# Performance work log

Hardware: AMD Instinct MI355X
Metric: run time of the kernel (lower is better)

The kernel has to match this reference:

```python
import jax, jax.numpy as jnp
import numpy as np

N, C, H, W = 32, 49, 9, 9   # batch, spectral bands (=outplane), spatial patch
MSIZE, K, PAD = 24, 7, 3    # conv3d out channels, spectral kernel, padding
EPS = 1e-5


def setup_inputs() -> dict:
    key = jax.random.key(0)
    k1, k2, k3 = jax.random.split(key, 3)
    x = jax.random.normal(k1, (N, C, H, W), dtype=jnp.float32)
    # Conv3d(1, MSIZE, [7,1,1]) params, PyTorch default uniform init
    fan_in = 1 * K * 1 * 1
    bound = 1.0 / np.sqrt(fan_in)
    conv_w = jax.random.uniform(k2, (MSIZE, 1, K, 1, 1), jnp.float32, -bound, bound)
    conv_b = jax.random.uniform(k3, (MSIZE,), jnp.float32, -bound, bound)
    # BatchNorm2d(49) affine params at init
    gamma = jnp.ones((C,), jnp.float32)
    beta = jnp.zeros((C,), jnp.float32)
    return {"x": x, "conv_w": conv_w, "conv_b": conv_b, "gamma": gamma, "beta": beta}


def reference(x, conv_w, conv_b, gamma, beta):
    n, c, h, w = x.shape
    # Conv3d over (depth=spectral, h, w) with kernel [K,1,1]: depth preserved
    x5 = x[:, None]  # (n,1,c,h,w)
    m = jax.lax.conv_general_dilated(
        x5, conv_w, window_strides=(1, 1, 1),
        padding=[(PAD, PAD), (0, 0), (0, 0)],
        dimension_numbers=("NCDHW", "OIDHW", "NCDHW"),
    ) + conv_b[None, :, None, None, None]        # (n, MSIZE, c, h, w)
    d = m.shape[1] * m.shape[2]                   # d = MSIZE * c
    mask = jax.nn.softmax(m.reshape(n, d, h * w), axis=-1).reshape(n, d, h, w)
    # original computes convm0 twice -> mask1 == mask0; reuse `mask` for both
    fk = jnp.einsum("ndhw,nchw->ncd", mask, x)    # (n, c, d)
    # out[n,c,h,w] = sum_d leaky_relu(fk[n,c,d] * mask[n,d,h,w])
    big = jnp.einsum("ncd,ndhw->ncdhw", fk, mask)  # (n,c,d,h,w) large intermediate
    out = jax.nn.leaky_relu(big, negative_slope=0.01).sum(axis=2)
    out = out + x                                  # residual
    # BatchNorm2d in training mode: batch statistics over (n,h,w) per channel
    mean = out.mean(axis=(0, 2, 3))
    var = out.var(axis=(0, 2, 3))
    out = (out - mean[:, None, None]) * jax.lax.rsqrt(var[:, None, None] + EPS)
    out = out * gamma[:, None, None] + beta[:, None, None]
    return out
```

## Files before the change

kernel.cpp:

```cpp
#include <hip/hip_runtime.h>
#include <hip/hip_bf16.h>

#define NN    32
#define CC    49
#define HWSZ  81
#define MSZ   24
#define KSZ   7
#define PADSZ 3
#define NHW   (NN*HWSZ)
#define NCHW  (NN*CC*HWSZ)

#define OPB   3
#define OGRP  (MSZ/OPB)

#define XSB_S  104
#define MSK_S  104
#define MSKT_S 72
#define G_S    72

typedef __attribute__((ext_vector_type(8))) short short8;
typedef __attribute__((ext_vector_type(4))) short short4v;
typedef __attribute__((ext_vector_type(4))) float f32x4;

__device__ __forceinline__ short f2b(float v) {
    unsigned u = __float_as_uint(v);
    u += 0x7fffu + ((u >> 16) & 1u);
    return (short)(u >> 16);
}
__device__ __forceinline__ float b2f(short s) {
    return __uint_as_float(((unsigned)(unsigned short)s) << 16);
}

__global__ __launch_bounds__(512) void fuse_k1(
    const float* __restrict__ x, const float* __restrict__ cw,
    const float* __restrict__ cb, float* __restrict__ acc)
{
    __shared__ short xsb [64 * XSB_S];
    __shared__ short msk [64 * MSK_S];
    __shared__ short mskT[96 * MSKT_S];
    __shared__ short gm  [64 * G_S];

    const int og = blockIdx.x;
    const int n  = blockIdx.y;
    const int t  = threadIdx.x;
    const int lane = t & 63;
    const int wv = t >> 6;
    const int lr = lane & 15;
    const int lq = lane >> 4;

    const float* xg = x + (size_t)n * CC * HWSZ;

    const f32x4 z4 = {0.f, 0.f, 0.f, 0.f};
    for (int i = t; i < CC * HWSZ; i += 512) {
        int c = i / HWSZ, hw = i - c * HWSZ;
        xsb[c * XSB_S + hw] = f2b(xg[i]);
    }
    if (t < CC) {
        short* row = xsb + t * XSB_S;
        #pragma unroll
        for (int cq = 81; cq < 88; ++cq) row[cq] = 0;
        *(f32x4*)(row + 88) = z4;
        *(f32x4*)(row + 96) = z4;
    }
    for (int j = t; j < 15 * 13; j += 512) {
        int rr = j / 13, cg = j - rr * 13;
        *(f32x4*)(xsb + (49 + rr) * XSB_S + cg * 8) = z4;
    }
    for (int i = t; i < 832; i += 512) ((f32x4*)msk)[i] = z4;
    for (int i = t; i < 864; i += 512) ((f32x4*)mskT)[i] = z4;
    __syncthreads();

    const int mt   = wv & 3;
    const int ntc0 = (wv >> 2) * 2;
    const int ct   = wv & 3;
    const int nh   = (wv >> 2) * 3;

    f32x4 dacc[3];
    #pragma unroll
    for (int j = 0; j < 3; ++j) dacc[j] = z4;

    for (int oo = 0; oo < OPB; ++oo) {
        const int o = og * OPB + oo;
        float wk[KSZ];
        #pragma unroll
        for (int k = 0; k < KSZ; ++k) wk[k] = cw[o * KSZ + k];
        const float bias = cb[o];

        #pragma unroll
        for (int it = 0; it < 2; ++it) {
            int dd = it * 32 + wv * 4 + lq;
            if (dd < CC) {
                float a0 = 0.f, a1 = 0.f, a2 = 0.f, a3 = 0.f, a4 = 0.f, a5 = 0.f;
                #pragma unroll
                for (int k = 0; k < KSZ; ++k) {
                    int r = dd + k - PADSZ;
                    if (r >= 0 && r < CC) {
                        const short* xr = xsb + r * XSB_S;
                        short4v xa = *(const short4v*)(xr + 4 * lr);
                        float w = wk[k];
                        a0 += w * b2f(xa[0]);
                        a1 += w * b2f(xa[1]);
                        a2 += w * b2f(xa[2]);
                        a3 += w * b2f(xa[3]);
                        a4 += w * b2f(xr[64 + lr]);
                        if (lr == 0) a5 += w * b2f(xr[80]);
                    }
                }
                float e0 = __expf(a0 + bias), e1 = __expf(a1 + bias);
                float e2 = __expf(a2 + bias), e3 = __expf(a3 + bias);
                float e4 = __expf(a4 + bias);
                float e5 = (lr == 0) ? __expf(a5 + bias) : 0.f;
                float s = ((e0 + e1) + (e2 + e3)) + (e4 + e5);
                #pragma unroll
                for (int off = 8; off; off >>= 1) s += __shfl_xor(s, off, 64);
                float inv = __builtin_amdgcn_rcpf(s);
                short4v pk;
                pk[0] = f2b(e0 * inv); pk[1] = f2b(e1 * inv);
                pk[2] = f2b(e2 * inv); pk[3] = f2b(e3 * inv);
                short b4 = f2b(e4 * inv);
                short* mrow = msk + dd * MSK_S;
                *(short4v*)(mrow + 4 * lr) = pk;
                mrow[64 + lr] = b4;
                mskT[(4 * lr    ) * MSKT_S + dd] = pk[0];
                mskT[(4 * lr + 1) * MSKT_S + dd] = pk[1];
                mskT[(4 * lr + 2) * MSKT_S + dd] = pk[2];
                mskT[(4 * lr + 3) * MSKT_S + dd] = pk[3];
                mskT[(64 + lr   ) * MSKT_S + dd] = b4;
                if (lr == 0) {
                    short b5 = f2b(e5 * inv);
                    mrow[80] = b5;
                    mskT[80 * MSKT_S + dd] = b5;
                }
            }
        }
        __syncthreads();

        {
            short8 a2f[3];
            #pragma unroll
            for (int ks = 0; ks < 3; ++ks)
                a2f[ks] = *(const short8*)&msk[(mt * 16 + lr) * MSK_S + ks * 32 + lq * 8];
            #pragma unroll
            for (int jn = 0; jn < 2; ++jn) {
                int nt = ntc0 + jn;
                f32x4 accv = {0.f, 0.f, 0.f, 0.f};
                #pragma unroll
                for (int ks = 0; ks < 3; ++ks) {
                    short8 b = *(const short8*)&xsb[(nt * 16 + lr) * XSB_S + ks * 32 + lq * 8];
                    accv = __builtin_amdgcn_mfma_f32_16x16x32_bf16(a2f[ks], b, accv, 0, 0, 0);
                }
                short4v pk;
                #pragma unroll
                for (int r = 0; r < 4; ++r) {
                    float v = accv[r];
                    v = (v >= 0.f) ? v : 0.01f * v;
                    pk[r] = f2b(v);
                }
                *(short4v*)&gm[(nt * 16 + lr) * G_S + mt * 16 + lq * 4] = pk;
            }
        }
        __syncthreads();

        {
            short8 a1f[2];
            #pragma unroll
            for (int ks = 0; ks < 2; ++ks)
                a1f[ks] = *(const short8*)&gm[(ct * 16 + lr) * G_S + ks * 32 + lq * 8];
            #pragma unroll
            for (int j = 0; j < 3; ++j) {
                int nt = nh + j;
                #pragma unroll
                for (int ks = 0; ks < 2; ++ks) {
                    short8 b = *(const short8*)&mskT[(nt * 16 + lr) * MSKT_S + ks * 32 + lq * 8];
                    dacc[j] = __builtin_amdgcn_mfma_f32_16x16x32_bf16(a1f[ks], b, dacc[j], 0, 0, 0);
                }
            }
        }
        __syncthreads();
    }

    float* dstn = acc + (size_t)n * CC * HWSZ;
    #pragma unroll
    for (int j = 0; j < 3; ++j) {
        int hw = (nh + j) * 16 + lr;
        if (hw < HWSZ) {
            int c0 = ct * 16 + lq * 4;
            #pragma unroll
            for (int r = 0; r < 4; ++r) {
                int c = c0 + r;
                if (c < CC) atomicAdd(dstn + c * HWSZ + hw, dacc[j][r]);
            }
        }
    }
}

__global__ __launch_bounds__(1024) void fuse_k2(
    float* __restrict__ out, const float* __restrict__ x,
    const float* __restrict__ gamma, const float* __restrict__ beta)
{
    const int c = blockIdx.x;
    const int t = threadIdx.x;
    float vals[3];
    float sum = 0.f, sq = 0.f;
    int cnt = 0;
    for (int i = t; i < NHW; i += 1024) {
        int n = i / HWSZ;
        int hw = i - n * HWSZ;
        int idx = (n * CC + c) * HWSZ + hw;
        float v = out[idx] + x[idx];
        vals[cnt++] = v;
        sum += v; sq += v * v;
    }
    #pragma unroll
    for (int off = 32; off; off >>= 1) {
        sum += __shfl_xor(sum, off, 64);
        sq  += __shfl_xor(sq, off, 64);
    }
    __shared__ float rs[16], rq[16];
    const int lane = t & 63, wv = t >> 6;
    if (lane == 0) { rs[wv] = sum; rq[wv] = sq; }
    __syncthreads();
    float ts = 0.f, tq = 0.f;
    #pragma unroll
    for (int w = 0; w < 16; ++w) { ts += rs[w]; tq += rq[w]; }
    const float invD = 1.f / (float)NHW;
    float mean = ts * invD;
    float var  = tq * invD - mean * mean;
    float scal = rsqrtf(var + 1e-5f) * gamma[c];
    float shft = beta[c] - mean * scal;
    cnt = 0;
    for (int i = t; i < NHW; i += 1024) {
        int n = i / HWSZ;
        int hw = i - n * HWSZ;
        out[(n * CC + c) * HWSZ + hw] = vals[cnt++] * scal + shft;
    }
}

extern "C" void kernel_launch(void* const* d_in, const int* in_sizes, int n_in,
                              void* d_out, int out_size, void* d_ws, size_t ws_size,
                              hipStream_t stream) {
    const float* x     = (const float*)d_in[0];
    const float* cw    = (const float*)d_in[1];
    const float* cb    = (const float*)d_in[2];
    const float* gamma = (const float*)d_in[3];
    const float* beta  = (const float*)d_in[4];
    float* out = (float*)d_out;

    hipMemsetAsync(out, 0, (size_t)NCHW * sizeof(float), stream);
    fuse_k1<<<dim3(OGRP, NN), 512, 0, stream>>>(x, cw, cb, out);
    fuse_k2<<<CC, 1024, 0, stream>>>(out, x, gamma, beta);
}
```

Before: 83.31 us.

## Fuse main and batchnorm kernels into one cooperative launch with per-channel blocks

Merges the two kernels into a single cooperative kernel that uses a grid-wide sync between the atomic accumulation and the batch-norm pass. It also changes the work split from 8 groups of 3 output channels with 512 threads to 24 single-channel blocks of 256 threads each. Each block now accumulates its partial result with atomics directly instead of looping over channels in registers. This adds parallelism (768 blocks) and removes one kernel launch, but requires all 768 blocks to be co-resident. It also multiplies atomics by 3 and x loads/conversions by 3, and the BN pass runs on only 49 blocks after the grid sync.

```diff
diff --git a/kernel.cpp b/kernel.cpp
--- a/kernel.cpp
+++ b/kernel.cpp
@@ -1,5 +1,8 @@
 #include <hip/hip_runtime.h>
 #include <hip/hip_bf16.h>
+#include <hip/hip_cooperative_groups.h>
+
+namespace cg = cooperative_groups;
 
 #define NN    32
 #define CC    49
@@ -10,9 +13,6 @@
 #define NHW   (NN*HWSZ)
 #define NCHW  (NN*CC*HWSZ)
 
-#define OPB   3
-#define OGRP  (MSZ/OPB)
-
 #define XSB_S  104
 #define MSK_S  104
 #define MSKT_S 72
@@ -31,27 +31,33 @@
     return __uint_as_float(((unsigned)(unsigned short)s) << 16);
 }
 
-__global__ __launch_bounds__(512) void fuse_k1(
+__global__ __launch_bounds__(256, 3) void fuse_all(
     const float* __restrict__ x, const float* __restrict__ cw,
-    const float* __restrict__ cb, float* __restrict__ acc)
+    const float* __restrict__ cb, const float* __restrict__ gamma,
+    const float* __restrict__ beta, float* __restrict__ out)
 {
     __shared__ short xsb [64 * XSB_S];
     __shared__ short msk [64 * MSK_S];
     __shared__ short mskT[96 * MSKT_S];
     __shared__ short gm  [64 * G_S];
-
-    const int og = blockIdx.x;
-    const int n  = blockIdx.y;
-    const int t  = threadIdx.x;
+    __shared__ float rs[4], rq[4];
+
+    const int o = blockIdx.x;
+    const int n = blockIdx.y;
+    const int t = threadIdx.x;
     const int lane = t & 63;
     const int wv = t >> 6;
     const int lr = lane & 15;
     const int lq = lane >> 4;
 
     const float* xg = x + (size_t)n * CC * HWSZ;
+    float wk[KSZ];
+    #pragma unroll
+    for (int k = 0; k < KSZ; ++k) wk[k] = cw[o * KSZ + k];
+    const float bias = cb[o];
 
     const f32x4 z4 = {0.f, 0.f, 0.f, 0.f};
-    for (int i = t; i < CC * HWSZ; i += 512) {
+    for (int i = t; i < CC * HWSZ; i += 256) {
         int c = i / HWSZ, hw = i - c * HWSZ;
         xsb[c * XSB_S + hw] = f2b(xg[i]);
     }
@@ -62,177 +68,150 @@
         *(f32x4*)(row + 88) = z4;
         *(f32x4*)(row + 96) = z4;
     }
-    for (int j = t; j < 15 * 13; j += 512) {
+    for (int j = t; j < 15 * 13; j += 256) {
         int rr = j / 13, cg = j - rr * 13;
         *(f32x4*)(xsb + (49 + rr) * XSB_S + cg * 8) = z4;
     }
-    for (int i = t; i < 832; i += 512) ((f32x4*)msk)[i] = z4;
-    for (int i = t; i < 864; i += 512) ((f32x4*)mskT)[i] = z4;
+    for (int i = t; i < 832; i += 256) ((f32x4*)msk)[i] = z4;
+    for (int i = t; i < 864; i += 256) ((f32x4*)mskT)[i] = z4;
     __syncthreads();
 
-    const int mt   = wv & 3;
-    const int ntc0 = (wv >> 2) * 2;
-    const int ct   = wv & 3;
-    const int nh   = (wv >> 2) * 3;
-
-    f32x4 dacc[3];
     #pragma unroll
-    for (int j = 0; j < 3; ++j) dacc[j] = z4;
-
-    for (int oo = 0; oo < OPB; ++oo) {
-        const int o = og * OPB + oo;
-        float wk[KSZ];
-        #pragma unroll
-        for (int k = 0; k < KSZ; ++k) wk[k] = cw[o * KSZ + k];
-        const float bias = cb[o];
-
-        #pragma unroll
-        for (int it = 0; it < 2; ++it) {
-            int dd = it * 32 + wv * 4 + lq;
-            if (dd < CC) {
-                float a0 = 0.f, a1 = 0.f, a2 = 0.f, a3 = 0.f, a4 = 0.f, a5 = 0.f;
-                #pragma unroll
-                for (int k = 0; k < KSZ; ++k) {
-                    int r = dd + k - PADSZ;
-                    if (r >= 0 && r < CC) {
-                        const short* xr = xsb + r * XSB_S;
-                        short4v xa = *(const short4v*)(xr + 4 * lr);
-                        float w = wk[k];
-                        a0 += w * b2f(xa[0]);
-                        a1 += w * b2f(xa[1]);
-                        a2 += w * b2f(xa[2]);
-                        a3 += w * b2f(xa[3]);
-                        a4 += w * b2f(xr[64 + lr]);
-                        if (lr == 0) a5 += w * b2f(xr[80]);
-                    }
+    for (int it = 0; it < 4; ++it) {
+        int dd = it * 16 + wv * 4 + lq;
+        if (dd < CC) {
+            float a0 = 0.f, a1 = 0.f, a2 = 0.f, a3 = 0.f, a4 = 0.f, a5 = 0.f;
+            #pragma unroll
+            for (int k = 0; k < KSZ; ++k) {
+                int r = dd + k - PADSZ;
+                if (r >= 0 && r < CC) {
+                    const short* xr = xsb + r * XSB_S;
+                    short4v xa = *(const short4v*)(xr + 4 * lr);
+                    float w = wk[k];
+                    a0 += w * b2f(xa[0]);
+                    a1 += w * b2f(xa[1]);
+                    a2 += w * b2f(xa[2]);
+                    a3 += w * b2f(xa[3]);
+                    a4 += w * b2f(xr[64 + lr]);
+                    if (lr == 0) a5 += w * b2f(xr[80]);
                 }
-                float e0 = __expf(a0 + bias), e1 = __expf(a1 + bias);
-                float e2 = __expf(a2 + bias), e3 = __expf(a3 + bias);
-                float e4 = __expf(a4 + bias);
-                float e5 = (lr == 0) ? __expf(a5 + bias) : 0.f;
-                float s = ((e0 + e1) + (e2 + e3)) + (e4 + e5);
-                #pragma unroll
-                for (int off = 8; off; off >>= 1) s += __shfl_xor(s, off, 64);
-                float inv = __builtin_amdgcn_rcpf(s);
-                short4v pk;
-                pk[0] = f2b(e0 * inv); pk[1] = f2b(e1 * inv);
-                pk[2] = f2b(e2 * inv); pk[3] = f2b(e3 * inv);
-                short b4 = f2b(e4 * inv);
-                short* mrow = msk + dd * MSK_S;
-                *(short4v*)(mrow + 4 * lr) = pk;
-                mrow[64 + lr] = b4;
-                mskT[(4 * lr    ) * MSKT_S + dd] = pk[0];
-                mskT[(4 * lr + 1) * MSKT_S + dd] = pk[1];
-                mskT[(4 * lr + 2) * MSKT_S + dd] = pk[2];
-                mskT[(4 * lr + 3) * MSKT_S + dd] = pk[3];
-                mskT[(64 + lr   ) * MSKT_S + dd] = b4;
-                if (lr == 0) {
-                    short b5 = f2b(e5 * inv);
-                    mrow[80] = b5;
-                    mskT[80 * MSKT_S + dd] = b5;
-                }
-            }
-        }
-        __syncthreads();
-
-        {
-            short8 a2f[3];
-            #pragma unroll
-            for (int ks = 0; ks < 3; ++ks)
-                a2f[ks] = *(const short8*)&msk[(mt * 16 + lr) * MSK_S + ks * 32 + lq * 8];
-            #pragma unroll
-            for (int jn = 0; jn < 2; ++jn) {
-                int nt = ntc0 + jn;
-                f32x4 accv = {0.f, 0.f, 0.f, 0.f};
-                #pragma unroll
-                for (int ks = 0; ks < 3; ++ks) {
-                    short8 b = *(const short8*)&xsb[(nt * 16 + lr) * XSB_S + ks * 32 + lq * 8];
-                    accv = __builtin_amdgcn_mfma_f32_16x16x32_bf16(a2f[ks], b, accv, 0, 0, 0);
-                }
-                short4v pk;
+            }
+            float e0 = __expf(a0 + bias), e1 = __expf(a1 + bias);
+            float e2 = __expf(a2 + bias), e3 = __expf(a3 + bias);
+            float e4 = __expf(a4 + bias);
+            float e5 = (lr == 0) ? __expf(a5 + bias) : 0.f;
+            float s = ((e0 + e1) + (e2 + e3)) + (e4 + e5);
+            #pragma unroll
+            for (int off = 8; off; off >>= 1) s += __shfl_xor(s, off, 64);
+            float inv = __builtin_amdgcn_rcpf(s);
+            short4v pk;
+            pk[0] = f2b(e0 * inv); pk[1] = f2b(e1 * inv);
+            pk[2] = f2b(e2 * inv); pk[3] = f2b(e3 * inv);
+            short b4 = f2b(e4 * inv);
+            short* mrow = msk + dd * MSK_S;
+            *(short4v*)(mrow + 4 * lr) = pk;
+            mrow[64 + lr] = b4;
+            mskT[(4 * lr    ) * MSKT_S + dd] = pk[0];
+            mskT[(4 * lr + 1) * MSKT_S + dd] = pk[1];
+            mskT[(4 * lr + 2) * MSKT_S + dd] = pk[2];
+            mskT[(4 * lr + 3) * MSKT_S + dd] = pk[3];
+            mskT[(64 + lr   ) * MSKT_S + dd] = b4;
+            if (lr == 0) {
+                short b5 = f2b(e5 * inv);
+                mrow[80] = b5;
+                mskT[80 * MSKT_S + dd] = b5;
+            }
+        }
+    }
+    __syncthreads();
+
+    {
+        short8 a2[3];
+        #pragma unroll
+        for (int ks = 0; ks < 3; ++ks)
+            a2[ks] = *(const short8*)&msk[(wv * 16 + lr) * MSK_S + ks * 32 + lq * 8];
+        #pragma unroll
+        for (int nt = 0; nt < 4; ++nt) {
+            f32x4 accv = {0.f, 0.f, 0.f, 0.f};
+            #pragma unroll
+            for (int ks = 0; ks < 3; ++ks) {
+                short8 b = *(const short8*)&xsb[(nt * 16 + lr) * XSB_S + ks * 32 + lq * 8];
+                accv = __builtin_amdgcn_mfma_f32_16x16x32_bf16(a2[ks], b, accv, 0, 0, 0);
+            }
+            short4v pk;
+            #pragma unroll
+            for (int r = 0; r < 4; ++r) {
+                float v = accv[r];
+                v = (v >= 0.f) ? v : 0.01f * v;
+                pk[r] = f2b(v);
+            }
+            *(short4v*)&gm[(nt * 16 + lr) * G_S + wv * 16 + lq * 4] = pk;
+        }
+    }
+    __syncthreads();
+
+    {
+        float* dstn = out + (size_t)n * CC * HWSZ;
+        short8 a1[2];
+        #pragma unroll
+        for (int ks = 0; ks < 2; ++ks)
+            a1[ks] = *(const short8*)&gm[(wv * 16 + lr) * G_S + ks * 32 + lq * 8];
+        #pragma unroll
+        for (int nt = 0; nt < 6; ++nt) {
+            f32x4 accv = {0.f, 0.f, 0.f, 0.f};
+            #pragma unroll
+            for (int ks = 0; ks < 2; ++ks) {
+                short8 b = *(const short8*)&mskT[(nt * 16 + lr) * MSKT_S + ks * 32 + lq * 8];
+                accv = __builtin_amdgcn_mfma_f32_16x16x32_bf16(a1[ks], b, accv, 0, 0, 0);
+            }
+            int hw = nt * 16 + lr;
+            if (hw < HWSZ) {
+                int cb4 = wv * 16 + lq * 4;
                 #pragma unroll
                 for (int r = 0; r < 4; ++r) {
-                    float v = accv[r];
-                    v = (v >= 0.f) ? v : 0.01f * v;
-                    pk[r] = f2b(v);
+                    int c = cb4 + r;
+                    if (c < CC) atomicAdd(dstn + c * HWSZ + hw, accv[r]);
                 }
-                *(short4v*)&gm[(nt * 16 + lr) * G_S + mt * 16 + lq * 4] = pk;
-            }
-        }
+            }
+        }
+    }
+
+    __threadfence();
+    cg::this_grid().sync();
+    __threadfence();
+
+    const int flat = blockIdx.y * MSZ + blockIdx.x;
+    if (flat < CC) {
+        const int c = flat;
+        float sum = 0.f, sq = 0.f;
+        for (int i = t; i < NHW; i += 256) {
+            int nn2 = i / HWSZ;
+            int hw = i - nn2 * HWSZ;
+            int idx = (nn2 * CC + c) * HWSZ + hw;
+            float v = out[idx] + x[idx];
+            sum += v; sq += v * v;
+        }
+        #pragma unroll
+        for (int off = 32; off; off >>= 1) {
+            sum += __shfl_xor(sum, off, 64);
+            sq  += __shfl_xor(sq, off, 64);
+        }
+        if (lane == 0) { rs[wv] = sum; rq[wv] = sq; }
         __syncthreads();
-
-        {
-            short8 a1f[2];
-            #pragma unroll
-            for (int ks = 0; ks < 2; ++ks)
-                a1f[ks] = *(const short8*)&gm[(ct * 16 + lr) * G_S + ks * 32 + lq * 8];
-            #pragma unroll
-            for (int j = 0; j < 3; ++j) {
-                int nt = nh + j;
-                #pragma unroll
-                for (int ks = 0; ks < 2; ++ks) {
-                    short8 b = *(const short8*)&mskT[(nt * 16 + lr) * MSKT_S + ks * 32 + lq * 8];
-                    dacc[j] = __builtin_amdgcn_mfma_f32_16x16x32_bf16(a1f[ks], b, dacc[j], 0, 0, 0);
-                }
-            }
-        }
-        __syncthreads();
-    }
-
-    float* dstn = acc + (size_t)n * CC * HWSZ;
-    #pragma unroll
-    for (int j = 0; j < 3; ++j) {
-        int hw = (nh + j) * 16 + lr;
-        if (hw < HWSZ) {
-            int c0 = ct * 16 + lq * 4;
-            #pragma unroll
-            for (int r = 0; r < 4; ++r) {
-                int c = c0 + r;
-                if (c < CC) atomicAdd(dstn + c * HWSZ + hw, dacc[j][r]);
-            }
-        }
-    }
-}
-
-__global__ __launch_bounds__(1024) void fuse_k2(
-    float* __restrict__ out, const float* __restrict__ x,
-    const float* __restrict__ gamma, const float* __restrict__ beta)
-{
-    const int c = blockIdx.x;
-    const int t = threadIdx.x;
-    float vals[3];
-    float sum = 0.f, sq = 0.f;
-    int cnt = 0;
-    for (int i = t; i < NHW; i += 1024) {
-        int n = i / HWSZ;
-        int hw = i - n * HWSZ;
-        int idx = (n * CC + c) * HWSZ + hw;
-        float v = out[idx] + x[idx];
-        vals[cnt++] = v;
-        sum += v; sq += v * v;
-    }
-    #pragma unroll
-    for (int off = 32; off; off >>= 1) {
-        sum += __shfl_xor(sum, off, 64);
-        sq  += __shfl_xor(sq, off, 64);
-    }
-    __shared__ float rs[16], rq[16];
-    const int lane = t & 63, wv = t >> 6;
-    if (lane == 0) { rs[wv] = sum; rq[wv] = sq; }
-    __syncthreads();
-    float ts = 0.f, tq = 0.f;
-    #pragma unroll
-    for (int w = 0; w < 16; ++w) { ts += rs[w]; tq += rq[w]; }
-    const float invD = 1.f / (float)NHW;
-    float mean = ts * invD;
-    float var  = tq * invD - mean * mean;
-    float scal = rsqrtf(var + 1e-5f) * gamma[c];
-    float shft = beta[c] - mean * scal;
-    cnt = 0;
-    for (int i = t; i < NHW; i += 1024) {
-        int n = i / HWSZ;
-        int hw = i - n * HWSZ;
-        out[(n * CC + c) * HWSZ + hw] = vals[cnt++] * scal + shft;
+        float ts = rs[0] + rs[1] + rs[2] + rs[3];
+        float tq = rq[0] + rq[1] + rq[2] + rq[3];
+        const float invD = 1.f / (float)NHW;
+        float mean = ts * invD;
+        float var  = tq * invD - mean * mean;
+        float scal = rsqrtf(var + 1e-5f) * gamma[c];
+        float shft = beta[c] - mean * scal;
+        for (int i = t; i < NHW; i += 256) {
+            int nn2 = i / HWSZ;
+            int hw = i - nn2 * HWSZ;
+            int idx = (nn2 * CC + c) * HWSZ + hw;
+            float v = out[idx] + x[idx];
+            out[idx] = v * scal + shft;
+        }
     }
 }
 
@@ -247,6 +226,9 @@
     float* out = (float*)d_out;
 
     hipMemsetAsync(out, 0, (size_t)NCHW * sizeof(float), stream);
-    fuse_k1<<<dim3(OGRP, NN), 512, 0, stream>>>(x, cw, cb, out);
-    fuse_k2<<<CC, 1024, 0, stream>>>(out, x, gamma, beta);
-}
+
+    void* args[] = {(void*)&x, (void*)&cw, (void*)&cb,
+                    (void*)&gamma, (void*)&beta, (void*)&out};
+    hipLaunchCooperativeKernel((const void*)fuse_all, dim3(MSZ, NN), dim3(256),
+                               args, 0, stream);
+}
```

Result: slower. 249.3 us (+199.3%).
